# Kernel optimization log

Hardware: AMD Instinct MI355X
Metric: run time of the kernel (lower is better)

The kernel has to match this reference:

```python
import jax, jax.numpy as jnp
import numpy as np

LMBDA = 1.0  # init lmbda

def setup_inputs() -> dict:
    key = jax.random.key(0)
    k1, k2, k3 = jax.random.split(key, 3)
    N, P, M = 8, 4096, 2048
    x_hat = jax.random.normal(k1, (N, P, 3), dtype=jnp.float32)
    points = jax.random.normal(k2, (N, P, 3), dtype=jnp.float32)
    # likelihoods in (0, 1]; avoid log2(0)
    lik_y = jax.random.uniform(k3, (N, M), dtype=jnp.float32, minval=1e-6, maxval=1.0)
    return {"x_hat": x_hat, "points": points, "lik_y": lik_y}

def _chamfer(x, y):
    # x: [N,P,3], y: [N,Q,3] -> scalar bidirectional mean chamfer (squared L2)
    x2 = jnp.sum(x * x, axis=-1)                      # [N,P]
    y2 = jnp.sum(y * y, axis=-1)                      # [N,Q]
    xy = jnp.einsum('npc,nqc->npq', x, y)             # [N,P,Q]
    d = x2[:, :, None] + y2[None if False else slice(None), None, :] - 2.0 * xy  # [N,P,Q]
    d = x2[:, :, None] + y2[:, None, :] - 2.0 * xy    # [N,P,Q] squared distances
    cham_x = jnp.mean(jnp.min(d, axis=2))             # x -> nearest in y
    cham_y = jnp.mean(jnp.min(d, axis=1))             # y -> nearest in x
    return cham_x + cham_y

def reference(x_hat, points, lik_y):
    N, P, C = points.shape
    # bpp loss: sum log2(likelihood) / (-N) bits, normalized per point
    bit_y = jnp.sum(jnp.log2(lik_y)) / (-N)
    bpp_y = bit_y / P
    bit_loss = bit_y
    bpp_loss = bit_loss / P
    rec_loss = _chamfer(x_hat, points)
    loss = bpp_loss + LMBDA * rec_loss
    return loss, bpp_loss, rec_loss, bit_loss, bpp_y
```

## Files before the change

### kernel.cpp

```cpp
#include <hip/hip_runtime.h>
#include <math.h>

#define NB 8
#define PP 4096
#define MM 2048
#define DIRS 2
#define QSLICES 16
#define QS (PP / QSLICES)
#define PCHUNK 1024
#define NPBLK (PP / PCHUNK)
#define NMIN (DIRS * NB * PP)
#define NLIK (NB * MM)

__global__ __launch_bounds__(256, 4) void chamfer_kernel(const float* __restrict__ x,
                                                         const float* __restrict__ y,
                                                         float* __restrict__ wspart) {
    int bx = blockIdx.x;
    int qs  = bx & (QSLICES - 1); bx >>= 4;
    int pc  = bx & (NPBLK - 1);   bx >>= 2;
    int n   = bx & (NB - 1);      bx >>= 3;
    int dir = bx;
    const float* a = dir ? y : x;
    const float* b = dir ? x : y;
    const float* an = a + (size_t)n * PP * 3;
    const float* bn = b + (size_t)n * PP * 3;

    __shared__ float4 lds[QS];
    int t = threadIdx.x;
    {
        int q = qs * QS + t;
        const float* bp = bn + (size_t)q * 3;
        float y0 = bp[0], y1 = bp[1], y2 = bp[2];
        lds[t] = make_float4(-2.f * y0, -2.f * y1, -2.f * y2,
                             y0 * y0 + y1 * y1 + y2 * y2);
    }

    float X0[4], X1[4], X2[4], XS[4], M[4];
    #pragma unroll
    for (int i = 0; i < 4; ++i) {
        int p = pc * PCHUNK + i * 256 + t;
        const float* ap = an + (size_t)p * 3;
        X0[i] = ap[0]; X1[i] = ap[1]; X2[i] = ap[2];
        XS[i] = X0[i] * X0[i] + X1[i] * X1[i] + X2[i] * X2[i];
        M[i] = INFINITY;
    }
    __syncthreads();

    #pragma unroll 4
    for (int q = 0; q < QS; q += 2) {
        float4 v0 = lds[q];
        float4 v1 = lds[q + 1];
        #pragma unroll
        for (int i = 0; i < 4; ++i) {
            float d0 = fmaf(X0[i], v0.x, fmaf(X1[i], v0.y, fmaf(X2[i], v0.z, v0.w)));
            float d1 = fmaf(X0[i], v1.x, fmaf(X1[i], v1.y, fmaf(X2[i], v1.z, v1.w)));
            M[i] = fminf(fminf(M[i], d0), d1);
        }
    }

    float* plane = wspart + (size_t)qs * NMIN;
    int slot = (dir * NB + n) * PP + pc * PCHUNK + t;
    #pragma unroll
    for (int i = 0; i < 4; ++i)
        plane[slot + i * 256] = M[i] + XS[i];
}

__global__ __launch_bounds__(256) void reduce_kernel(const float* __restrict__ wspart,
                                                     const float* __restrict__ lik,
                                                     float* __restrict__ wssum,
                                                     float* __restrict__ out) {
    int t = blockIdx.x * 256 + threadIdx.x;
    float m = wspart[t];
    #pragma unroll
    for (int s = 1; s < QSLICES; ++s)
        m = fminf(m, wspart[(size_t)s * NMIN + t]);

    float l = 0.f;
    if (t < NLIK) l = __log2f(lik[t]);

    #pragma unroll
    for (int off = 32; off > 0; off >>= 1) {
        m += __shfl_down(m, off, 64);
        l += __shfl_down(l, off, 64);
    }
    __shared__ float rm[4], rl[4];
    int lane = threadIdx.x & 63, wid = threadIdx.x >> 6;
    if (lane == 0) { rm[wid] = m; rl[wid] = l; }
    __syncthreads();
    if (threadIdx.x == 0) {
        int dir = blockIdx.x >> 7;
        atomicAdd(&wssum[dir], rm[0] + rm[1] + rm[2] + rm[3]);
        if (blockIdx.x < 64)
            atomicAdd(&wssum[2], rl[0] + rl[1] + rl[2] + rl[3]);
        __threadfence();
        unsigned done = atomicAdd((unsigned*)&wssum[3], 1u);
        if (done == 255u) {
            __threadfence();
            float s0 = __hip_atomic_load(&wssum[0], __ATOMIC_ACQUIRE, __HIP_MEMORY_SCOPE_AGENT);
            float s1 = __hip_atomic_load(&wssum[1], __ATOMIC_ACQUIRE, __HIP_MEMORY_SCOPE_AGENT);
            float s2 = __hip_atomic_load(&wssum[2], __ATOMIC_ACQUIRE, __HIP_MEMORY_SCOPE_AGENT);
            float rec = s0 / (float)(NB * PP) + s1 / (float)(NB * PP);
            float bit_y = s2 / (-(float)NB);
            float bpp = bit_y / (float)PP;
            out[0] = bpp + 1.0f * rec;
            out[1] = bpp;
            out[2] = rec;
            out[3] = bit_y;
            out[4] = bpp;
        }
    }
}

extern "C" void kernel_launch(void* const* d_in, const int* in_sizes, int n_in,
                              void* d_out, int out_size, void* d_ws, size_t ws_size,
                              hipStream_t stream) {
    const float* x_hat  = (const float*)d_in[0];
    const float* points = (const float*)d_in[1];
    const float* lik    = (const float*)d_in[2];
    float* out = (float*)d_out;
    float* wssum  = (float*)d_ws;
    float* wspart = (float*)d_ws + 16;

    hipMemsetAsync(wssum, 0, 16, stream);
    chamfer_kernel<<<DIRS * NB * NPBLK * QSLICES, 256, 0, stream>>>(x_hat, points, wspart);
    reduce_kernel<<<256, 256, 0, stream>>>(wspart, lik, wssum, out);
}
```

Baseline: 41.48 us.

## Use packed FP32 FMA over paired query points with larger per-thread tile

Reorganizes the LDS layout so each pair of query points is stored as interleaved two-wide vectors, which lets the distance computation use packed two-lane FMA (v_pk_fma_f32) and process two queries per instruction. Each thread now holds 8 source points instead of 4, which halves the block count and raises register reuse of every LDS load. The goal is fewer VALU instructions per distance. The cost is higher register pressure, lower occupancy (launch bounds reduced to 2) and fewer blocks to fill the GPU.

New measurement: 41.08 us. About the same (-1.0%).

```diff
diff --git a/kernel.cpp b/kernel.cpp
--- a/kernel.cpp
+++ b/kernel.cpp
@@ -7,17 +7,20 @@
 #define DIRS 2
 #define QSLICES 16
 #define QS (PP / QSLICES)
-#define PCHUNK 1024
+#define NPTS 8
+#define PCHUNK (256 * NPTS)
 #define NPBLK (PP / PCHUNK)
 #define NMIN (DIRS * NB * PP)
 #define NLIK (NB * MM)
 
-__global__ __launch_bounds__(256, 4) void chamfer_kernel(const float* __restrict__ x,
+typedef float v2f __attribute__((ext_vector_type(2)));
+
+__global__ __launch_bounds__(256, 2) void chamfer_kernel(const float* __restrict__ x,
                                                          const float* __restrict__ y,
                                                          float* __restrict__ wspart) {
     int bx = blockIdx.x;
     int qs  = bx & (QSLICES - 1); bx >>= 4;
-    int pc  = bx & (NPBLK - 1);   bx >>= 2;
+    int pc  = bx & (NPBLK - 1);   bx >>= 1;
     int n   = bx & (NB - 1);      bx >>= 3;
     int dir = bx;
     const float* a = dir ? y : x;
@@ -25,43 +28,51 @@
     const float* an = a + (size_t)n * PP * 3;
     const float* bn = b + (size_t)n * PP * 3;
 
-    __shared__ float4 lds[QS];
+    __shared__ float4 lds[QS * 2 / 2 * 2];
     int t = threadIdx.x;
-    {
-        int q = qs * QS + t;
-        const float* bp = bn + (size_t)q * 3;
-        float y0 = bp[0], y1 = bp[1], y2 = bp[2];
-        lds[t] = make_float4(-2.f * y0, -2.f * y1, -2.f * y2,
-                             y0 * y0 + y1 * y1 + y2 * y2);
-    }
 
-    float X0[4], X1[4], X2[4], XS[4], M[4];
+    float X0[NPTS], X1[NPTS], X2[NPTS], XS[NPTS], M[NPTS];
     #pragma unroll
-    for (int i = 0; i < 4; ++i) {
+    for (int i = 0; i < NPTS; ++i) {
         int p = pc * PCHUNK + i * 256 + t;
         const float* ap = an + (size_t)p * 3;
         X0[i] = ap[0]; X1[i] = ap[1]; X2[i] = ap[2];
         XS[i] = X0[i] * X0[i] + X1[i] * X1[i] + X2[i] * X2[i];
         M[i] = INFINITY;
     }
+
+    {
+        int q = qs * QS + t;
+        const float* bp = bn + (size_t)q * 3;
+        float y0 = bp[0], y1 = bp[1], y2 = bp[2];
+        int j = t >> 1, par = t & 1;
+        float* base = (float*)&lds[2 * j];
+        base[0 + par] = -2.f * y0;
+        base[2 + par] = -2.f * y1;
+        base[4 + par] = -2.f * y2;
+        base[6 + par] = y0 * y0 + y1 * y1 + y2 * y2;
+    }
     __syncthreads();
 
-    #pragma unroll 4
-    for (int q = 0; q < QS; q += 2) {
-        float4 v0 = lds[q];
-        float4 v1 = lds[q + 1];
+    #pragma unroll 2
+    for (int j = 0; j < QS / 2; ++j) {
+        float4 A = lds[2 * j];
+        float4 B = lds[2 * j + 1];
+        v2f Y0 = {A.x, A.y}, Y1 = {A.z, A.w}, Y2 = {B.x, B.y}, YS = {B.z, B.w};
         #pragma unroll
-        for (int i = 0; i < 4; ++i) {
-            float d0 = fmaf(X0[i], v0.x, fmaf(X1[i], v0.y, fmaf(X2[i], v0.z, v0.w)));
-            float d1 = fmaf(X0[i], v1.x, fmaf(X1[i], v1.y, fmaf(X2[i], v1.z, v1.w)));
-            M[i] = fminf(fminf(M[i], d0), d1);
+        for (int i = 0; i < NPTS; ++i) {
+            v2f x0 = {X0[i], X0[i]}, x1 = {X1[i], X1[i]}, x2 = {X2[i], X2[i]};
+            v2f d = __builtin_elementwise_fma(x0, Y0,
+                    __builtin_elementwise_fma(x1, Y1,
+                    __builtin_elementwise_fma(x2, Y2, YS)));
+            M[i] = fminf(fminf(M[i], d.x), d.y);
         }
     }
 
     float* plane = wspart + (size_t)qs * NMIN;
     int slot = (dir * NB + n) * PP + pc * PCHUNK + t;
     #pragma unroll
-    for (int i = 0; i < 4; ++i)
+    for (int i = 0; i < NPTS; ++i)
         plane[slot + i * 256] = M[i] + XS[i];
 }
 
```
